# Performance work log

Hardware: AMD Instinct MI355X
Metric: run time of the kernel (lower is better)

The kernel has to match this reference:

```python
import jax, jax.numpy as jnp
import numpy as np


def _to_box_list(x):
    # (batch, ch, nw, nh) -> (nw*nh, batch, ch)  [convert_to_box_list]
    b, c, nw, nh = x.shape
    return jnp.transpose(x, (2, 3, 0, 1)).reshape(nw * nh, b, c)


def _bilinear_sample(img, px, py):
    # img: (ch, X, Y); px: (Sx,), py: (Sy,) pixel coords; zero padding outside.
    ch, X, Y = img.shape
    x0 = jnp.floor(px); y0 = jnp.floor(py)
    wx = px - x0; wy = py - y0
    x0i = x0.astype(jnp.int32); y0i = y0.astype(jnp.int32)
    def g(xi, yi):
        xc = jnp.clip(xi, 0, X - 1); yc = jnp.clip(yi, 0, Y - 1)
        v = img[:, xc[:, None], yc[None, :]]
        m = (((xi >= 0) & (xi < X))[:, None] & ((yi >= 0) & (yi < Y))[None, :]).astype(img.dtype)
        return v * m
    return ((1 - wx)[:, None] * ((1 - wy)[None, :] * g(x0i, y0i) + wy[None, :] * g(x0i, y0i + 1))
            + wx[:, None] * ((1 - wy)[None, :] * g(x0i + 1, y0i) + wy[None, :] * g(x0i + 1, y0i + 1)))


def setup_inputs():
    key = jax.random.key(0)
    ks = jax.random.split(key, 12)
    B, CH_IN, W, H = 8, 1, 256, 256
    NW = NH = 32
    DZW, DZI, FCH, S = 4, 16, 32, 28
    feat_flat = FCH * S * S   # 25088
    out_flat = (CH_IN + 1) * S * S  # 1568
    return {
        "imgs_in": jax.random.uniform(ks[0], (B, CH_IN, W, H), jnp.float32),
        "features": jax.random.normal(ks[1], (B, FCH, W, H), jnp.float32),
        "zwhere_mu": jax.random.normal(ks[2], (B, DZW, NW, NH), jnp.float32),
        "zwhere_std": jax.random.uniform(ks[3], (B, DZW, NW, NH), jnp.float32) * 0.9 + 0.1,
        "logit_mu": jax.random.normal(ks[4], (B, 1, NW, NH), jnp.float32),
        "w_zwhere": jax.random.normal(ks[5], (4, DZW), jnp.float32) * 0.5,
        "b_zwhere": jnp.zeros((4,), jnp.float32),
        "w_enc_mu": jax.random.normal(ks[6], (DZI, feat_flat), jnp.float32) * 0.01,
        "b_enc_mu": jnp.zeros((DZI,), jnp.float32),
        "w_enc_std": jax.random.normal(ks[7], (DZI, feat_flat), jnp.float32) * 0.01,
        "b_enc_std": jnp.zeros((DZI,), jnp.float32),
        "w_dec": jax.random.normal(ks[8], (out_flat, DZI), jnp.float32) * 0.1,
        "b_dec": jnp.zeros((out_flat,), jnp.float32),
        "n_objects_max": 25,
        "cropped_size": 28,
        "size_min": 24,
        "size_max": 96,
    }


def reference(imgs_in, features, zwhere_mu, zwhere_std, logit_mu,
              w_zwhere, b_zwhere, w_enc_mu, b_enc_mu, w_enc_std, b_enc_std,
              w_dec, b_dec, n_objects_max, cropped_size, size_min, size_max):
    B, CH_IN, W, H = imgs_in.shape
    S = cropped_size
    eps = 1e-8

    # ---- box decode: Decoder1by1Linear (1x1 conv) + sigmoid + tmaps_to_bb ----
    tmaps = jax.nn.sigmoid(jnp.einsum('bcwh,oc->bowh', zwhere_mu, w_zwhere)
                           + b_zwhere[None, :, None, None])
    tx, ty, tw, th = tmaps[:, 0], tmaps[:, 1], tmaps[:, 2], tmaps[:, 3]  # (B, nw, nh)
    nw, nh = tx.shape[-2], tx.shape[-1]
    ix = jnp.arange(nw, dtype=tx.dtype)[:, None]
    iy = jnp.arange(nh, dtype=tx.dtype)[None, :]
    def tolist2(m):  # (B, nw, nh) -> (nw*nh, B)
        return jnp.transpose(m, (1, 2, 0)).reshape(nw * nh, B)
    bx_all = tolist2(W * (ix + tx) / nw)
    by_all = tolist2(H * (iy + ty) / nh)
    bw_all = tolist2(size_min + (size_max - size_min) * tw)
    bh_all = tolist2(size_min + (size_max - size_min) * th)

    # ---- prob map, Bernoulli KL vs prior 0.5, deterministic top-k (topk_only NMS) ----
    p_map = jax.nn.sigmoid(logit_mu)                                     # c_map.sample
    kl_logit = (jnp.log(2.0) + p_map * jnp.log(p_map + eps)
                + (1 - p_map) * jnp.log(1 - p_map + eps))               # c_map.kl
    p_list = _to_box_list(p_map)[..., 0]        # (n_all, B)
    logit_list = _to_box_list(logit_mu)[..., 0]
    _, idx_bk = jax.lax.top_k(p_list.T, n_objects_max)  # (B, k)
    index_top_k = idx_bk.T                              # (k, B)

    c_few = jnp.take_along_axis(p_list, index_top_k, axis=0)
    logit_few = jnp.take_along_axis(logit_list, index_top_k, axis=0)
    bx = jnp.take_along_axis(bx_all, index_top_k, axis=0)
    by = jnp.take_along_axis(by_all, index_top_k, axis=0)
    bw = jnp.take_along_axis(bw_all, index_top_k, axis=0)
    bh = jnp.take_along_axis(bh_all, index_top_k, axis=0)

    # ---- zwhere KL (diag normal vs N(0,1)), gathered at top-k boxes ----
    kl_zwhere_map = 0.5 * (zwhere_std ** 2 + zwhere_mu ** 2 - 1.0) - jnp.log(zwhere_std)
    kl_zwhere_all = _to_box_list(kl_zwhere_map)          # (n_all, B, dz)
    idx3 = jnp.broadcast_to(index_top_k[:, :, None],
                            (n_objects_max, B, kl_zwhere_all.shape[-1]))
    kl_zwhere_few = jnp.take_along_axis(kl_zwhere_all, idx3, axis=0)

    # ---- Cropper.crop: bilinear crop of UNet features at selected boxes ----
    def crop_one(img, cx, cy, cw, chh):
        t = jnp.arange(S, dtype=img.dtype) / (S - 1)
        return _bilinear_sample(img, cx - 0.5 * cw + t * cw, cy - 0.5 * chh + t * chh)
    crop_boxes = jax.vmap(crop_one, in_axes=(None, 0, 0, 0, 0))
    crop_all = jax.vmap(crop_boxes, in_axes=(0, 1, 1, 1, 1), out_axes=1)
    cropped = crop_all(features, bx, by, bw, bh)  # (k, B, FCH, S, S)

    # ---- encoder_zinstance -> z sample (= mu, noisy_sampling=False) + KL ----
    xf = cropped.reshape(n_objects_max, B, -1)
    z_mu = xf @ w_enc_mu.T + b_enc_mu
    z_std = jax.nn.softplus(xf @ w_enc_std.T + b_enc_std)
    z_sample = z_mu
    kl_zinstance = 0.5 * (z_std ** 2 + z_mu ** 2 - 1.0) - jnp.log(z_std + eps)

    # ---- decoder_zinstance -> small stuff: softplus weight ch, sigmoid img ch ----
    small_raw = (z_sample @ w_dec.T + b_dec).reshape(n_objects_max, B, CH_IN + 1, S, S)
    small = jnp.concatenate([jax.nn.softplus(small_raw[..., :1, :, :]),
                             jax.nn.sigmoid(small_raw[..., 1:, :, :])], axis=-3)

    # ---- Uncropper.uncrop: paste each small patch back at its box location ----
    def uncrop_one(sm, cx, cy, cw, chh):
        u = jnp.arange(W, dtype=sm.dtype)
        v = jnp.arange(H, dtype=sm.dtype)
        sx = (u - (cx - 0.5 * cw)) / cw * (S - 1)
        sy = (v - (cy - 0.5 * chh)) / chh * (S - 1)
        return _bilinear_sample(sm, sx, sy)
    big_stuff = jax.vmap(jax.vmap(uncrop_one))(small, bx, by, bw, bh)  # (k,B,2,W,H)

    big_weight = big_stuff[..., :1, :, :]
    big_img = big_stuff[..., 1:, :, :]
    sum_w = jnp.sum(big_weight, axis=0, keepdims=True)  # dim=-5 is box dim
    big_mask = jnp.tanh(sum_w) * (big_weight / jnp.clip(sum_w, 1e-6))
    big_mask_non = jnp.tanh(big_weight)

    return (logit_mu, logit_few, big_mask, big_mask_non, big_img,
            p_map, c_few, bx, by, bw, bh, z_sample,
            kl_logit, kl_zwhere_few, kl_zinstance)
```

## Files before the change

### kernel.cpp

```cpp
#include <hip/hip_runtime.h>
#include <math.h>

#define B 8
#define FCH 32
#define WI 256
#define HI 256
#define NW 32
#define NH 32
#define NBOX 1024
#define K 25
#define S 28
#define DZI 16
#define FEAT_FLAT (FCH*S*S)
#define FEAT4 (FEAT_FLAT/4)
#define OUT_FLAT (2*S*S)
#define SMIN 24.0f
#define SMAX 96.0f
#define BIG_SZ (K*B*WI*HI)

#define NCHUNK 49
#define CH4 128

#define O_LOGIT_MU    0
#define O_LOGIT_FEW   8192
#define O_BIG_MASK    8392
#define O_BIG_MASK_NON (O_BIG_MASK + BIG_SZ)
#define O_BIG_IMG     (O_BIG_MASK_NON + BIG_SZ)
#define O_P_MAP       (O_BIG_IMG + BIG_SZ)
#define O_C_FEW       (O_P_MAP + 8192)
#define O_BX          (O_C_FEW + 200)
#define O_BY          (O_BX + 200)
#define O_BW          (O_BY + 200)
#define O_BH          (O_BW + 200)
#define O_Z_SAMPLE    (O_BH + 200)
#define O_KL_LOGIT    (O_Z_SAMPLE + 3200)
#define O_KL_ZWHERE   (O_KL_LOGIT + 8192)
#define O_KL_ZINST    (O_KL_ZWHERE + 800)

__device__ __forceinline__ float sigmoidf_(float x) { return 1.0f / (1.0f + expf(-x)); }
__device__ __forceinline__ float softplusf_(float x) { return fmaxf(x, 0.0f) + log1pf(expf(-fabsf(x))); }
__device__ __forceinline__ float sig_fast(float x) { return 1.0f / (1.0f + __expf(-x)); }
__device__ __forceinline__ float sp_fast(float x)  { return fmaxf(x, 0.0f) + __logf(1.0f + __expf(-fabsf(x))); }
__device__ __forceinline__ float tanh_fast(float x) {
    float e = __expf(-2.0f * x);
    return (1.0f - e) / (1.0f + e);
}

__device__ __forceinline__ float tap256(const float* img, int x, int y) {
    bool in = ((unsigned)x < 256u) && ((unsigned)y < 256u);
    int xc = min(max(x, 0), 255), yc = min(max(y, 0), 255);
    float v = img[xc * 256 + yc];
    return in ? v : 0.0f;
}

__device__ __forceinline__ float tap28(const float* img, int x, int y) {
    bool in = ((unsigned)x < 28u) && ((unsigned)y < 28u);
    int xc = min(max(x, 0), 27), yc = min(max(y, 0), 27);
    float v = img[xc * 28 + yc];
    return in ? v : 0.0f;
}

__global__ void topk_misc_kernel(const float* __restrict__ logit_mu,
                                 const float* __restrict__ zmu, const float* __restrict__ zstd,
                                 const float* __restrict__ w_zw, const float* __restrict__ b_zw,
                                 float* __restrict__ out, float* __restrict__ ws_boxes) {
    int b = blockIdx.x;
    int lane = threadIdx.x;
    const float* lg = logit_mu + b * NBOX;
    float vals[16];
    #pragma unroll
    for (int m = 0; m < 16; ++m) vals[m] = lg[m * 64 + lane];

    #pragma unroll
    for (int m = 0; m < 16; ++m) {
        int idx = b * NBOX + m * 64 + lane;
        float x = vals[m];
        out[O_LOGIT_MU + idx] = x;
        float p = sigmoidf_(x);
        out[O_P_MAP + idx] = p;
        out[O_KL_LOGIT + idx] = 0.69314718055994531f + p * logf(p + 1e-8f) + (1.0f - p) * logf(1.0f - p + 1e-8f);
    }

    unsigned taken = 0;
    int sel_idx = 0;
    for (int ks = 0; ks < K; ++ks) {
        float bv = -INFINITY; int bi = 0x7fffffff;
        #pragma unroll
        for (int m = 0; m < 16; ++m) {
            if (!(taken & (1u << m))) {
                float v = vals[m]; int idx = m * 64 + lane;
                if (v > bv || (v == bv && idx < bi)) { bv = v; bi = idx; }
            }
        }
        #pragma unroll
        for (int sh = 32; sh >= 1; sh >>= 1) {
            float ov = __shfl_xor(bv, sh);
            int   oi = __shfl_xor(bi, sh);
            if (ov > bv || (ov == bv && oi < bi)) { bv = ov; bi = oi; }
        }
        if ((bi & 63) == lane) taken |= (1u << (bi >> 6));
        if (lane == ks) sel_idx = bi;
        if (lane == 0) {
            out[O_LOGIT_FEW + ks * B + b] = bv;
            out[O_C_FEW + ks * B + b] = sigmoidf_(bv);
        }
    }

    if (lane < K) {
        int idx = sel_idx;
        int w = idx >> 5, h = idx & 31;
        float mu_c[4];
        #pragma unroll
        for (int c = 0; c < 4; ++c) mu_c[c] = zmu[((b * 4 + c) * NW + w) * NH + h];
        float t[4];
        #pragma unroll
        for (int o = 0; o < 4; ++o) {
            float a = b_zw[o];
            #pragma unroll
            for (int c = 0; c < 4; ++c) a = fmaf(mu_c[c], w_zw[o * 4 + c], a);
            t[o] = sigmoidf_(a);
        }
        float bx = (float)WI * ((float)w + t[0]) / (float)NW;
        float by = (float)HI * ((float)h + t[1]) / (float)NH;
        float bw = SMIN + (SMAX - SMIN) * t[2];
        float bh = SMIN + (SMAX - SMIN) * t[3];
        int kb = lane * B + b;
        out[O_BX + kb] = bx;
        out[O_BY + kb] = by;
        out[O_BW + kb] = bw;
        out[O_BH + kb] = bh;
        ((float4*)ws_boxes)[kb] = make_float4(bx, by, bw, bh);
        #pragma unroll
        for (int c = 0; c < 4; ++c) {
            float m = mu_c[c];
            float sd = zstd[((b * 4 + c) * NW + w) * NH + h];
            out[O_KL_ZWHERE + kb * 4 + c] = 0.5f * (sd * sd + m * m - 1.0f) - logf(sd);
        }
    }
}

__device__ __forceinline__ void csample4(const float* __restrict__ fb, int i4,
                                         float x_lo, float y_lo, float swx, float swy,
                                         float v[4]) {
    int i = i4 << 2;
    unsigned c = (unsigned)i / 784u;
    unsigned s = (unsigned)i - c * 784u;
    unsigned ix = s / 28u;
    unsigned iy = s - ix * 28u;
    const float* img = fb + (size_t)c * (WI * HI);
    float px = fmaf((float)ix, swx, x_lo);
    float x0f = floorf(px); float fx = px - x0f; int x0 = (int)x0f;
    #pragma unroll
    for (int q = 0; q < 4; ++q) {
        float py = fmaf((float)(iy + q), swy, y_lo);
        float y0f = floorf(py); float fy = py - y0f; int y0 = (int)y0f;
        float a00 = tap256(img, x0, y0),     a01 = tap256(img, x0, y0 + 1);
        float a10 = tap256(img, x0 + 1, y0), a11 = tap256(img, x0 + 1, y0 + 1);
        v[q] = (1.0f - fx) * ((1.0f - fy) * a00 + fy * a01)
             +         fx  * ((1.0f - fy) * a10 + fy * a11);
    }
}

__global__ __launch_bounds__(128) void crop_writer_kernel(
        const float* __restrict__ features, const float* __restrict__ ws_boxes,
        float* __restrict__ crop) {
    int kb = blockIdx.y;
    int i4 = blockIdx.x * 128 + threadIdx.x;
    int b = kb & 7;
    float4 box = ((const float4*)ws_boxes)[kb];
    float x_lo = box.x - 0.5f * box.z, y_lo = box.y - 0.5f * box.w;
    float swx = box.z * (1.0f / 27.0f), swy = box.w * (1.0f / 27.0f);
    const float* fb = features + (size_t)b * (FCH * WI * HI);
    float v[4];
    csample4(fb, i4, x_lo, y_lo, swx, swy, v);
    ((float4*)crop)[(size_t)kb * FEAT4 + i4] = make_float4(v[0], v[1], v[2], v[3]);
}

__device__ __forceinline__ float dot4f(float4 v, float4 w, float a) {
    return fmaf(v.x, w.x, fmaf(v.y, w.y, fmaf(v.z, w.z, fmaf(v.w, w.w, a))));
}

__global__ __launch_bounds__(512) void enc_gemm_kernel(
        const float* __restrict__ crop,
        const float* __restrict__ w_mu, const float* __restrict__ w_std,
        float* __restrict__ ws_part) {
    int blk = blockIdx.x;
    int g = blk / NCHUNK, chunk = blk - g * NCHUNK;
    int wave = threadIdx.x >> 6, lane = threadIdx.x & 63;
    int base4 = chunk * CH4;
    const float4* cp4 = (const float4*)crop;

    __shared__ float4 crop_lds[8][CH4];
    {
        int t1 = threadIdx.x, t2 = threadIdx.x + 512;
        crop_lds[t1 >> 7][t1 & 127] = cp4[(size_t)(g * 8 + (t1 >> 7)) * FEAT4 + base4 + (t1 & 127)];
        crop_lds[t2 >> 7][t2 & 127] = cp4[(size_t)(g * 8 + (t2 >> 7)) * FEAT4 + base4 + (t2 & 127)];
    }

    int row = wave * 4;
    const float4* wsrc = (row < 16) ? ((const float4*)w_mu + (size_t)row * FEAT4)
                                    : ((const float4*)w_std + (size_t)(row - 16) * FEAT4);
    int i4a = base4 + lane, i4b = i4a + 64;
    float4 wa[4], wb[4];
    #pragma unroll
    for (int r = 0; r < 4; ++r) {
        wa[r] = wsrc[(size_t)r * FEAT4 + i4a];
        wb[r] = wsrc[(size_t)r * FEAT4 + i4b];
    }

    float cur[32];
    #pragma unroll
    for (int j = 0; j < 32; ++j) cur[j] = 0.0f;

    __syncthreads();

    #pragma unroll
    for (int bb = 0; bb < 8; ++bb) {
        float4 ca = crop_lds[bb][lane];
        float4 cb = crop_lds[bb][lane + 64];
        #pragma unroll
        for (int r = 0; r < 4; ++r)
            cur[r * 8 + bb] = dot4f(cb, wb[r], dot4f(ca, wa[r], cur[r * 8 + bb]));
    }

    {   bool bit = (lane & 1) != 0; float nx[16];
        #pragma unroll
        for (int j = 0; j < 16; ++j) {
            float keep = bit ? cur[2*j+1] : cur[2*j];
            float send = bit ? cur[2*j]   : cur[2*j+1];
            nx[j] = keep + __shfl_xor(send, 1);
        }
        #pragma unroll
        for (int j = 0; j < 16; ++j) cur[j] = nx[j];
    }
    {   bool bit = (lane & 2) != 0; float nx[8];
        #pragma unroll
        for (int j = 0; j < 8; ++j) {
            float keep = bit ? cur[2*j+1] : cur[2*j];
            float send = bit ? cur[2*j]   : cur[2*j+1];
            nx[j] = keep + __shfl_xor(send, 2);
        }
        #pragma unroll
        for (int j = 0; j < 8; ++j) cur[j] = nx[j];
    }
    {   bool bit = (lane & 4) != 0; float nx[4];
        #pragma unroll
        for (int j = 0; j < 4; ++j) {
            float keep = bit ? cur[2*j+1] : cur[2*j];
            float send = bit ? cur[2*j]   : cur[2*j+1];
            nx[j] = keep + __shfl_xor(send, 4);
        }
        #pragma unroll
        for (int j = 0; j < 4; ++j) cur[j] = nx[j];
    }
    {   bool bit = (lane & 8) != 0; float nx[2];
        #pragma unroll
        for (int j = 0; j < 2; ++j) {
            float keep = bit ? cur[2*j+1] : cur[2*j];
            float send = bit ? cur[2*j]   : cur[2*j+1];
            nx[j] = keep + __shfl_xor(send, 8);
        }
        cur[0] = nx[0]; cur[1] = nx[1];
    }
    {   bool bit = (lane & 16) != 0;
        float keep = bit ? cur[1] : cur[0];
        float send = bit ? cur[0] : cur[1];
        cur[0] = keep + __shfl_xor(send, 16);
    }
    float tot = cur[0] + __shfl_xor(cur[0], 32);
    if (lane < 32) {
        int kbx = g * 8 + (lane & 7);
        ws_part[((size_t)kbx * NCHUNK + chunk) * 32 + row + (lane >> 3)] = tot;
    }
}

__global__ __launch_bounds__(256) void dec_enc_kernel(
        const float* __restrict__ ws_part,
        const float* __restrict__ b_mu, const float* __restrict__ b_std,
        const float* __restrict__ w_dec, const float* __restrict__ b_dec,
        float* __restrict__ ws_small, float* __restrict__ out) {
    int kb = blockIdx.x;
    int t = threadIdx.x;
    __shared__ float zsh[DZI], spsh[DZI];
    if (t < 32) {
        float s = 0.0f;
        for (int c = 0; c < NCHUNK; ++c) s += ws_part[((size_t)kb * NCHUNK + c) * 32 + t];
        if (t < DZI) zsh[t] = s + b_mu[t];
        else         spsh[t - DZI] = s + b_std[t - DZI];
    }
    __syncthreads();
    if (t < DZI) {
        float m = zsh[t];
        float sd = softplusf_(spsh[t]);
        out[O_Z_SAMPLE + kb * DZI + t] = m;
        out[O_KL_ZINST + kb * DZI + t] = 0.5f * (sd * sd + m * m - 1.0f) - logf(sd + 1e-8f);
    }
    float z[DZI];
    #pragma unroll
    for (int j = 0; j < DZI; ++j) z[j] = zsh[j];
    for (int o = t; o < OUT_FLAT; o += 256) {
        const float4* wd = (const float4*)(w_dec + o * DZI);
        float4 w0 = wd[0], w1 = wd[1], w2 = wd[2], w3 = wd[3];
        float a = b_dec[o];
        a = fmaf(z[0], w0.x, fmaf(z[1], w0.y, fmaf(z[2], w0.z, fmaf(z[3], w0.w, a))));
        a = fmaf(z[4], w1.x, fmaf(z[5], w1.y, fmaf(z[6], w1.z, fmaf(z[7], w1.w, a))));
        a = fmaf(z[8], w2.x, fmaf(z[9], w2.y, fmaf(z[10], w2.z, fmaf(z[11], w2.w, a))));
        a = fmaf(z[12], w3.x, fmaf(z[13], w3.y, fmaf(z[14], w3.z, fmaf(z[15], w3.w, a))));
        float r = (o < 784) ? sp_fast(a) : sig_fast(a);
        ws_small[(size_t)kb * OUT_FLAT + o] = r;
    }
}

__device__ __forceinline__ void sample4_wi(const float* __restrict__ p0, float sx,
                                           float y_lo, float ih, int v0,
                                           float* __restrict__ w, float* __restrict__ im) {
    const float* p1 = p0 + 784;
    float x0f = floorf(sx); float fx = sx - x0f; int x0 = (int)x0f;
    #pragma unroll
    for (int q = 0; q < 4; ++q) {
        float sy = ((float)(v0 + q) - y_lo) * ih;
        float wv = 0.0f, iv = 0.0f;
        if (sy > -1.0f && sy < 28.0f) {
            float y0f = floorf(sy); float fy = sy - y0f; int y0 = (int)y0f;
            float a00 = tap28(p0, x0, y0),     a01 = tap28(p0, x0, y0 + 1);
            float a10 = tap28(p0, x0 + 1, y0), a11 = tap28(p0, x0 + 1, y0 + 1);
            wv = (1.0f - fx) * ((1.0f - fy) * a00 + fy * a01)
               +         fx  * ((1.0f - fy) * a10 + fy * a11);
            float c00 = tap28(p1, x0, y0),     c01 = tap28(p1, x0, y0 + 1);
            float c10 = tap28(p1, x0 + 1, y0), c11 = tap28(p1, x0 + 1, y0 + 1);
            iv = (1.0f - fx) * ((1.0f - fy) * c00 + fy * c01)
               +         fx  * ((1.0f - fy) * c10 + fy * c11);
        }
        w[q] = wv; im[q] = iv;
    }
}

__device__ __forceinline__ void sample4_w(const float* __restrict__ p0, float sx,
                                          float y_lo, float ih, int v0,
                                          float* __restrict__ w) {
    float x0f = floorf(sx); float fx = sx - x0f; int x0 = (int)x0f;
    #pragma unroll
    for (int q = 0; q < 4; ++q) {
        float sy = ((float)(v0 + q) - y_lo) * ih;
        float wv = 0.0f;
        if (sy > -1.0f && sy < 28.0f) {
            float y0f = floorf(sy); float fy = sy - y0f; int y0 = (int)y0f;
            float a00 = tap28(p0, x0, y0),     a01 = tap28(p0, x0, y0 + 1);
            float a10 = tap28(p0, x0 + 1, y0), a11 = tap28(p0, x0 + 1, y0 + 1);
            wv = (1.0f - fx) * ((1.0f - fy) * a00 + fy * a01)
               +         fx  * ((1.0f - fy) * a10 + fy * a11);
        }
        w[q] = wv;
    }
}

__global__ __launch_bounds__(256) void uncrop_kernel(const float* __restrict__ ws_small,
                                                     const float* __restrict__ ws_boxes,
                                                     float* __restrict__ out) {
    int blk = blockIdx.x;
    int b = blk >> 6;
    int u0 = (blk & 63) << 2;
    int t = threadIdx.x;
    int u = u0 + (t >> 6);
    int v0 = (t & 63) << 2;

    __shared__ float4 bt[K];
    if (t < K) {
        float4 bx = ((const float4*)ws_boxes)[t * B + b];
        bt[t] = make_float4(bx.x - 0.5f * bx.z, bx.y - 0.5f * bx.w, 27.0f / bx.z, 27.0f / bx.w);
    }
    __syncthreads();

    float fu = (float)u;
    float sum[4] = {0.0f, 0.0f, 0.0f, 0.0f};
    #pragma unroll 2
    for (int k = 0; k < K; ++k) {
        float4 bb = bt[k];
        float sx = (fu - bb.x) * bb.z;
        float w[4] = {0, 0, 0, 0}, im[4] = {0, 0, 0, 0};
        if (sx > -1.0f && sx < 28.0f) {
            const float* p0 = ws_small + (size_t)(k * B + b) * OUT_FLAT;
            sample4_wi(p0, sx, bb.y, bb.w, v0, w, im);
        }
        #pragma unroll
        for (int q = 0; q < 4; ++q) sum[q] += w[q];
        size_t base = (((size_t)(k * B + b) * 256 + u) * 256 + v0);
        *(float4*)(out + O_BIG_IMG + base) = make_float4(im[0], im[1], im[2], im[3]);
        *(float4*)(out + O_BIG_MASK_NON + base) =
            make_float4(tanh_fast(w[0]), tanh_fast(w[1]), tanh_fast(w[2]), tanh_fast(w[3]));
    }
    float sc[4];
    #pragma unroll
    for (int q = 0; q < 4; ++q) sc[q] = tanh_fast(sum[q]) / fmaxf(sum[q], 1e-6f);
    #pragma unroll 2
    for (int k = 0; k < K; ++k) {
        float4 bb = bt[k];
        float sx = (fu - bb.x) * bb.z;
        float w[4] = {0, 0, 0, 0};
        if (sx > -1.0f && sx < 28.0f) {
            const float* p0 = ws_small + (size_t)(k * B + b) * OUT_FLAT;
            sample4_w(p0, sx, bb.y, bb.w, v0, w);
        }
        size_t base = (((size_t)(k * B + b) * 256 + u) * 256 + v0);
        *(float4*)(out + O_BIG_MASK + base) =
            make_float4(w[0] * sc[0], w[1] * sc[1], w[2] * sc[2], w[3] * sc[3]);
    }
}

extern "C" void kernel_launch(void* const* d_in, const int* in_sizes, int n_in,
                              void* d_out, int out_size, void* d_ws, size_t ws_size,
                              hipStream_t stream) {
    const float* features = (const float*)d_in[1];
    const float* zwhere_mu = (const float*)d_in[2];
    const float* zwhere_std = (const float*)d_in[3];
    const float* logit_mu = (const float*)d_in[4];
    const float* w_zwhere = (const float*)d_in[5];
    const float* b_zwhere = (const float*)d_in[6];
    const float* w_enc_mu = (const float*)d_in[7];
    const float* b_enc_mu = (const float*)d_in[8];
    const float* w_enc_std = (const float*)d_in[9];
    const float* b_enc_std = (const float*)d_in[10];
    const float* w_dec = (const float*)d_in[11];
    const float* b_dec = (const float*)d_in[12];
    float* out = (float*)d_out;

    float* ws_boxes = (float*)d_ws;
    float* ws_part  = ws_boxes + 200 * 4;
    float* ws_small = ws_part + 200 * NCHUNK * 32;
    float* ws_crop  = out + O_BIG_IMG;

    hipLaunchKernelGGL(topk_misc_kernel, dim3(B), dim3(64), 0, stream,
                       logit_mu, zwhere_mu, zwhere_std, w_zwhere, b_zwhere, out, ws_boxes);
    hipLaunchKernelGGL(crop_writer_kernel, dim3(49, 200), dim3(128), 0, stream,
                       features, ws_boxes, ws_crop);
    hipLaunchKernelGGL(enc_gemm_kernel, dim3(25 * NCHUNK), dim3(512), 0, stream,
                       ws_crop, w_enc_mu, w_enc_std, ws_part);
    hipLaunchKernelGGL(dec_enc_kernel, dim3(K * B), dim3(256), 0, stream,
                       ws_part, b_enc_mu, b_enc_std, w_dec, b_dec, ws_small, out);
    hipLaunchKernelGGL(uncrop_kernel, dim3(B * 64), dim3(256), 0, stream,
                       ws_small, ws_boxes, out);
}
```

Before: 128.8 us.

## Fuse crop sampling into encoder GEMM, drop intermediate crop buffer

The separate crop_writer kernel is removed. Each encoder GEMM block now bilinearly samples its own 8 boxes × 128-float4 chunk of features straight into LDS instead of reading a precomputed crop tensor from global memory. This saves one kernel launch and the write and re-read of a roughly 20 MB crop buffer that lived in the output area. In exchange, the sampling work now runs inside the 512-thread GEMM blocks and can add latency to them, though each crop element is still computed exactly once.

```diff
diff --git a/kernel.cpp b/kernel.cpp
--- a/kernel.cpp
+++ b/kernel.cpp
@@ -139,6 +139,10 @@
     }
 }
 
+__device__ __forceinline__ float dot4f(float4 v, float4 w, float a) {
+    return fmaf(v.x, w.x, fmaf(v.y, w.y, fmaf(v.z, w.z, fmaf(v.w, w.w, a))));
+}
+
 __device__ __forceinline__ void csample4(const float* __restrict__ fb, int i4,
                                          float x_lo, float y_lo, float swx, float swy,
                                          float v[4]) {
@@ -161,41 +165,16 @@
     }
 }
 
-__global__ __launch_bounds__(128) void crop_writer_kernel(
-        const float* __restrict__ features, const float* __restrict__ ws_boxes,
-        float* __restrict__ crop) {
-    int kb = blockIdx.y;
-    int i4 = blockIdx.x * 128 + threadIdx.x;
-    int b = kb & 7;
-    float4 box = ((const float4*)ws_boxes)[kb];
-    float x_lo = box.x - 0.5f * box.z, y_lo = box.y - 0.5f * box.w;
-    float swx = box.z * (1.0f / 27.0f), swy = box.w * (1.0f / 27.0f);
-    const float* fb = features + (size_t)b * (FCH * WI * HI);
-    float v[4];
-    csample4(fb, i4, x_lo, y_lo, swx, swy, v);
-    ((float4*)crop)[(size_t)kb * FEAT4 + i4] = make_float4(v[0], v[1], v[2], v[3]);
-}
-
-__device__ __forceinline__ float dot4f(float4 v, float4 w, float a) {
-    return fmaf(v.x, w.x, fmaf(v.y, w.y, fmaf(v.z, w.z, fmaf(v.w, w.w, a))));
-}
-
-__global__ __launch_bounds__(512) void enc_gemm_kernel(
-        const float* __restrict__ crop,
+__global__ __launch_bounds__(512) void crop_gemm_kernel(
+        const float* __restrict__ features,
         const float* __restrict__ w_mu, const float* __restrict__ w_std,
-        float* __restrict__ ws_part) {
+        const float* __restrict__ ws_boxes, float* __restrict__ ws_part) {
     int blk = blockIdx.x;
     int g = blk / NCHUNK, chunk = blk - g * NCHUNK;
     int wave = threadIdx.x >> 6, lane = threadIdx.x & 63;
     int base4 = chunk * CH4;
-    const float4* cp4 = (const float4*)crop;
 
     __shared__ float4 crop_lds[8][CH4];
-    {
-        int t1 = threadIdx.x, t2 = threadIdx.x + 512;
-        crop_lds[t1 >> 7][t1 & 127] = cp4[(size_t)(g * 8 + (t1 >> 7)) * FEAT4 + base4 + (t1 & 127)];
-        crop_lds[t2 >> 7][t2 & 127] = cp4[(size_t)(g * 8 + (t2 >> 7)) * FEAT4 + base4 + (t2 & 127)];
-    }
 
     int row = wave * 4;
     const float4* wsrc = (row < 16) ? ((const float4*)w_mu + (size_t)row * FEAT4)
@@ -206,6 +185,21 @@
     for (int r = 0; r < 4; ++r) {
         wa[r] = wsrc[(size_t)r * FEAT4 + i4a];
         wb[r] = wsrc[(size_t)r * FEAT4 + i4b];
+    }
+
+    #pragma unroll
+    for (int pass = 0; pass < 2; ++pass) {
+        int gidx = threadIdx.x + pass * 512;
+        int bb = gidx >> 7;
+        int e  = gidx & 127;
+        int kb = g * 8 + bb;
+        float4 box = ((const float4*)ws_boxes)[kb];
+        float x_lo = box.x - 0.5f * box.z, y_lo = box.y - 0.5f * box.w;
+        float swx = box.z * (1.0f / 27.0f), swy = box.w * (1.0f / 27.0f);
+        const float* fb = features + (size_t)(kb & 7) * (FCH * WI * HI);
+        float v[4];
+        csample4(fb, base4 + e, x_lo, y_lo, swx, swy, v);
+        crop_lds[bb][e] = make_float4(v[0], v[1], v[2], v[3]);
     }
 
     float cur[32];
@@ -427,14 +421,11 @@
     float* ws_boxes = (float*)d_ws;
     float* ws_part  = ws_boxes + 200 * 4;
     float* ws_small = ws_part + 200 * NCHUNK * 32;
-    float* ws_crop  = out + O_BIG_IMG;
 
     hipLaunchKernelGGL(topk_misc_kernel, dim3(B), dim3(64), 0, stream,
                        logit_mu, zwhere_mu, zwhere_std, w_zwhere, b_zwhere, out, ws_boxes);
-    hipLaunchKernelGGL(crop_writer_kernel, dim3(49, 200), dim3(128), 0, stream,
-                       features, ws_boxes, ws_crop);
-    hipLaunchKernelGGL(enc_gemm_kernel, dim3(25 * NCHUNK), dim3(512), 0, stream,
-                       ws_crop, w_enc_mu, w_enc_std, ws_part);
+    hipLaunchKernelGGL(crop_gemm_kernel, dim3(25 * NCHUNK), dim3(512), 0, stream,
+                       features, w_enc_mu, w_enc_std, ws_boxes, ws_part);
     hipLaunchKernelGGL(dec_enc_kernel, dim3(K * B), dim3(256), 0, stream,
                        ws_part, b_enc_mu, b_enc_std, w_dec, b_dec, ws_small, out);
     hipLaunchKernelGGL(uncrop_kernel, dim3(B * 64), dim3(256), 0, stream,
```

Result: faster. 125.7 us (-2.4%).

## Stage crop source window in LDS and halve per-thread uncrop work

Applied to the files above, without the earlier changes.

The crop kernel now assigns one block per (channel, box), loads the bounding window of the source feature map into shared memory with coalesced reads, and does the bilinear taps from LDS. Before, each thread did four scattered global gathers per output. The uncrop kernel now handles two columns per thread instead of four, doubling the grid to raise parallelism at the cost of narrower float2 stores. The LDS buffer is sized for boxes up to about 98x98 pixels, which depends on the maximum box size.

```diff
diff --git a/kernel.cpp b/kernel.cpp
--- a/kernel.cpp
+++ b/kernel.cpp
@@ -46,13 +46,6 @@
     return (1.0f - e) / (1.0f + e);
 }
 
-__device__ __forceinline__ float tap256(const float* img, int x, int y) {
-    bool in = ((unsigned)x < 256u) && ((unsigned)y < 256u);
-    int xc = min(max(x, 0), 255), yc = min(max(y, 0), 255);
-    float v = img[xc * 256 + yc];
-    return in ? v : 0.0f;
-}
-
 __device__ __forceinline__ float tap28(const float* img, int x, int y) {
     bool in = ((unsigned)x < 28u) && ((unsigned)y < 28u);
     int xc = min(max(x, 0), 27), yc = min(max(y, 0), 27);
@@ -139,41 +132,53 @@
     }
 }
 
-__device__ __forceinline__ void csample4(const float* __restrict__ fb, int i4,
-                                         float x_lo, float y_lo, float swx, float swy,
-                                         float v[4]) {
-    int i = i4 << 2;
-    unsigned c = (unsigned)i / 784u;
-    unsigned s = (unsigned)i - c * 784u;
-    unsigned ix = s / 28u;
-    unsigned iy = s - ix * 28u;
-    const float* img = fb + (size_t)c * (WI * HI);
-    float px = fmaf((float)ix, swx, x_lo);
-    float x0f = floorf(px); float fx = px - x0f; int x0 = (int)x0f;
-    #pragma unroll
-    for (int q = 0; q < 4; ++q) {
-        float py = fmaf((float)(iy + q), swy, y_lo);
-        float y0f = floorf(py); float fy = py - y0f; int y0 = (int)y0f;
-        float a00 = tap256(img, x0, y0),     a01 = tap256(img, x0, y0 + 1);
-        float a10 = tap256(img, x0 + 1, y0), a11 = tap256(img, x0 + 1, y0 + 1);
-        v[q] = (1.0f - fx) * ((1.0f - fy) * a00 + fy * a01)
-             +         fx  * ((1.0f - fy) * a10 + fy * a11);
-    }
-}
-
-__global__ __launch_bounds__(128) void crop_writer_kernel(
+__global__ __launch_bounds__(256) void crop_writer_kernel(
         const float* __restrict__ features, const float* __restrict__ ws_boxes,
         float* __restrict__ crop) {
+    int c  = blockIdx.x;
     int kb = blockIdx.y;
-    int i4 = blockIdx.x * 128 + threadIdx.x;
-    int b = kb & 7;
+    int b  = kb & 7;
     float4 box = ((const float4*)ws_boxes)[kb];
     float x_lo = box.x - 0.5f * box.z, y_lo = box.y - 0.5f * box.w;
     float swx = box.z * (1.0f / 27.0f), swy = box.w * (1.0f / 27.0f);
-    const float* fb = features + (size_t)b * (FCH * WI * HI);
-    float v[4];
-    csample4(fb, i4, x_lo, y_lo, swx, swy, v);
-    ((float4*)crop)[(size_t)kb * FEAT4 + i4] = make_float4(v[0], v[1], v[2], v[3]);
+    int x0min = (int)floorf(x_lo);
+    int y0min = (int)floorf(y_lo);
+    int nx = (int)floorf(fmaf(27.0f, swx, x_lo)) + 2 - x0min;
+    int ny = (int)floorf(fmaf(27.0f, swy, y_lo)) + 2 - y0min;
+    int nyp = ny + 1;
+    const float* img = features + ((size_t)b * FCH + c) * (WI * HI);
+
+    __shared__ float lds[9800];
+
+    int t = threadIdx.x;
+    for (int r = (t >> 6); r < nx; r += 4) {
+        int gx = x0min + r;
+        int gxc = min(max(gx, 0), 255);
+        bool xin = (unsigned)gx < 256u;
+        for (int cc = (t & 63); cc < ny; cc += 64) {
+            int gy = y0min + cc;
+            int gyc = min(max(gy, 0), 255);
+            float v = img[gxc * 256 + gyc];
+            bool in = xin && ((unsigned)gy < 256u);
+            lds[r * nyp + cc] = in ? v : 0.0f;
+        }
+    }
+    __syncthreads();
+
+    float* dst = crop + (size_t)kb * FEAT_FLAT + c * 784;
+    for (int s = t; s < 784; s += 256) {
+        int ix = s / 28;
+        int iy = s - ix * 28;
+        float px = fmaf((float)ix, swx, x_lo);
+        float py = fmaf((float)iy, swy, y_lo);
+        float x0f = floorf(px), y0f = floorf(py);
+        float fx = px - x0f, fy = py - y0f;
+        int xr = (int)x0f - x0min, yr = (int)y0f - y0min;
+        const float* p = lds + xr * nyp + yr;
+        float a00 = p[0], a01 = p[1], a10 = p[nyp], a11 = p[nyp + 1];
+        dst[s] = (1.0f - fx) * ((1.0f - fy) * a00 + fy * a01)
+               +         fx  * ((1.0f - fy) * a10 + fy * a11);
+    }
 }
 
 __device__ __forceinline__ float dot4f(float4 v, float4 w, float a) {
@@ -311,13 +316,13 @@
     }
 }
 
-__device__ __forceinline__ void sample4_wi(const float* __restrict__ p0, float sx,
+__device__ __forceinline__ void sample2_wi(const float* __restrict__ p0, float sx,
                                            float y_lo, float ih, int v0,
                                            float* __restrict__ w, float* __restrict__ im) {
     const float* p1 = p0 + 784;
     float x0f = floorf(sx); float fx = sx - x0f; int x0 = (int)x0f;
     #pragma unroll
-    for (int q = 0; q < 4; ++q) {
+    for (int q = 0; q < 2; ++q) {
         float sy = ((float)(v0 + q) - y_lo) * ih;
         float wv = 0.0f, iv = 0.0f;
         if (sy > -1.0f && sy < 28.0f) {
@@ -335,12 +340,12 @@
     }
 }
 
-__device__ __forceinline__ void sample4_w(const float* __restrict__ p0, float sx,
+__device__ __forceinline__ void sample2_w(const float* __restrict__ p0, float sx,
                                           float y_lo, float ih, int v0,
                                           float* __restrict__ w) {
     float x0f = floorf(sx); float fx = sx - x0f; int x0 = (int)x0f;
     #pragma unroll
-    for (int q = 0; q < 4; ++q) {
+    for (int q = 0; q < 2; ++q) {
         float sy = ((float)(v0 + q) - y_lo) * ih;
         float wv = 0.0f;
         if (sy > -1.0f && sy < 28.0f) {
@@ -358,11 +363,11 @@
                                                      const float* __restrict__ ws_boxes,
                                                      float* __restrict__ out) {
     int blk = blockIdx.x;
-    int b = blk >> 6;
-    int u0 = (blk & 63) << 2;
+    int b = blk >> 7;
+    int ug = blk & 127;
     int t = threadIdx.x;
-    int u = u0 + (t >> 6);
-    int v0 = (t & 63) << 2;
+    int u = ug * 2 + (t >> 7);
+    int v0 = (t & 127) << 1;
 
     __shared__ float4 bt[K];
     if (t < K) {
@@ -372,38 +377,35 @@
     __syncthreads();
 
     float fu = (float)u;
-    float sum[4] = {0.0f, 0.0f, 0.0f, 0.0f};
+    float sum[2] = {0.0f, 0.0f};
     #pragma unroll 2
     for (int k = 0; k < K; ++k) {
         float4 bb = bt[k];
         float sx = (fu - bb.x) * bb.z;
-        float w[4] = {0, 0, 0, 0}, im[4] = {0, 0, 0, 0};
+        float w[2] = {0, 0}, im[2] = {0, 0};
         if (sx > -1.0f && sx < 28.0f) {
             const float* p0 = ws_small + (size_t)(k * B + b) * OUT_FLAT;
-            sample4_wi(p0, sx, bb.y, bb.w, v0, w, im);
-        }
-        #pragma unroll
-        for (int q = 0; q < 4; ++q) sum[q] += w[q];
+            sample2_wi(p0, sx, bb.y, bb.w, v0, w, im);
+        }
+        sum[0] += w[0]; sum[1] += w[1];
         size_t base = (((size_t)(k * B + b) * 256 + u) * 256 + v0);
-        *(float4*)(out + O_BIG_IMG + base) = make_float4(im[0], im[1], im[2], im[3]);
-        *(float4*)(out + O_BIG_MASK_NON + base) =
-            make_float4(tanh_fast(w[0]), tanh_fast(w[1]), tanh_fast(w[2]), tanh_fast(w[3]));
-    }
-    float sc[4];
-    #pragma unroll
-    for (int q = 0; q < 4; ++q) sc[q] = tanh_fast(sum[q]) / fmaxf(sum[q], 1e-6f);
+        *(float2*)(out + O_BIG_IMG + base) = make_float2(im[0], im[1]);
+        *(float2*)(out + O_BIG_MASK_NON + base) = make_float2(tanh_fast(w[0]), tanh_fast(w[1]));
+    }
+    float sc[2];
+    sc[0] = tanh_fast(sum[0]) / fmaxf(sum[0], 1e-6f);
+    sc[1] = tanh_fast(sum[1]) / fmaxf(sum[1], 1e-6f);
     #pragma unroll 2
     for (int k = 0; k < K; ++k) {
         float4 bb = bt[k];
         float sx = (fu - bb.x) * bb.z;
-        float w[4] = {0, 0, 0, 0};
+        float w[2] = {0, 0};
         if (sx > -1.0f && sx < 28.0f) {
             const float* p0 = ws_small + (size_t)(k * B + b) * OUT_FLAT;
-            sample4_w(p0, sx, bb.y, bb.w, v0, w);
+            sample2_w(p0, sx, bb.y, bb.w, v0, w);
         }
         size_t base = (((size_t)(k * B + b) * 256 + u) * 256 + v0);
-        *(float4*)(out + O_BIG_MASK + base) =
-            make_float4(w[0] * sc[0], w[1] * sc[1], w[2] * sc[2], w[3] * sc[3]);
+        *(float2*)(out + O_BIG_MASK + base) = make_float2(w[0] * sc[0], w[1] * sc[1]);
     }
 }
 
@@ -431,12 +433,12 @@
 
     hipLaunchKernelGGL(topk_misc_kernel, dim3(B), dim3(64), 0, stream,
                        logit_mu, zwhere_mu, zwhere_std, w_zwhere, b_zwhere, out, ws_boxes);
-    hipLaunchKernelGGL(crop_writer_kernel, dim3(49, 200), dim3(128), 0, stream,
+    hipLaunchKernelGGL(crop_writer_kernel, dim3(FCH, 200), dim3(256), 0, stream,
                        features, ws_boxes, ws_crop);
     hipLaunchKernelGGL(enc_gemm_kernel, dim3(25 * NCHUNK), dim3(512), 0, stream,
                        ws_crop, w_enc_mu, w_enc_std, ws_part);
     hipLaunchKernelGGL(dec_enc_kernel, dim3(K * B), dim3(256), 0, stream,
                        ws_part, b_enc_mu, b_enc_std, w_dec, b_dec, ws_small, out);
-    hipLaunchKernelGGL(uncrop_kernel, dim3(B * 64), dim3(256), 0, stream,
+    hipLaunchKernelGGL(uncrop_kernel, dim3(B * 128), dim3(256), 0, stream,
                        ws_small, ws_boxes, out);
 }
```

Measured after the change: 155.5 us. 20.8% more time.
